# Optimization experiments

Hardware: AMD Instinct MI355X
Metric: run time of the kernel (lower is better)

## Reference

```python
import jax, jax.numpy as jnp
import numpy as np

B, I, H, O, K = 256, 512, 512, 512, 256


def setup_inputs() -> dict:
    key = jax.random.key(0)
    ks = jax.random.split(key, 16)
    def lin(kw, kb, out_dim, in_dim):
        s = 1.0 / np.sqrt(in_dim)
        W = jax.random.uniform(kw, (out_dim, in_dim), jnp.float32, -s, s)
        b = jax.random.uniform(kb, (out_dim,), jnp.float32, -s, s)
        return W, b
    Wd, bd = lin(ks[0], ks[1], H, I + 2 * H)
    Wr, br = lin(ks[2], ks[3], H, I + H)
    Wz, bz = lin(ks[4], ks[5], H, I + H)
    Wh, bh = lin(ks[6], ks[7], H, I + H)
    Wo, bo = lin(ks[8], ks[9], O, H)
    return {
        "sample": jax.random.normal(ks[10], (B, I), jnp.float32),
        "hidden": jax.random.normal(ks[11], (B, H), jnp.float32),
        "hidden_tensor": jax.random.normal(ks[12], (K, B, H), jnp.float32),
        "d_0": jax.random.normal(ks[13], (B, H), jnp.float32),
        "Wd": Wd, "bd": bd, "Wr": Wr, "br": br,
        "Wz": Wz, "bz": bz, "Wh": Wh, "bh": bh, "Wo": Wo, "bo": bo,
    }


def _filter_d(hidden_tensor, d_values):
    # get_ws: w[j] = prod_{m=0}^{K-1-j} (m - d) / (m + 1)  for j in [0, K)
    # Vectorized: cumprod of (m-d)/(m+1) along m, then flip.
    m = jnp.arange(K, dtype=d_values.dtype).reshape(K, 1, 1)  # [K,1,1]
    factors = (m - d_values[None, :, :]) / (m + 1.0)          # [K,B,H]
    w = jnp.flip(jnp.cumprod(factors, axis=0), axis=0)        # [K,B,H]
    return jnp.sum(hidden_tensor * w, axis=0)                 # [B,H]


def reference(sample, hidden, hidden_tensor, d_0,
              Wd, bd, Wr, br, Wz, bz, Wh, bh, Wo, bo):
    combined = jnp.concatenate([sample, hidden], axis=1)          # [B, I+H]
    combined_d = jnp.concatenate([sample, hidden, d_0], axis=1)   # [B, I+2H]

    d_values = jax.nn.sigmoid(combined_d @ Wd.T + bd) * 0.5       # [B,H]
    first = -_filter_d(hidden_tensor, d_values)                   # [B,H]

    r_gate = jax.nn.sigmoid(combined @ Wr.T + br)
    z_gate = jax.nn.sigmoid(combined @ Wz.T + bz)

    combined2 = jnp.concatenate([sample, r_gate * hidden], axis=1)
    h_tilde = jnp.tanh(combined2 @ Wh.T + bh)
    second = h_tilde * (1.0 - z_gate)

    hidden_new = first + second                                   # [B,H]
    h_c_1 = jnp.concatenate([hidden_tensor, hidden_new[None]], axis=0)[1:]  # [K,B,H]
    output = hidden_new @ Wo.T + bo                               # [B,O]
    return (output, hidden_new, h_c_1, d_values)
```

## Files before the change

### kernel.cpp

```cpp
#include <hip/hip_runtime.h>

#define B_ 256
#define H_ 512
#define KF 256
#define BH 131072
#define BH4 32768
#define H4 128

#define BM 64
#define BN 64
#define BK 16

__device__ __forceinline__ float sigmoidf_(float x) { return 1.0f / (1.0f + __expf(-x)); }
__device__ __forceinline__ float tanh_fast(float x) { return 2.0f / (1.0f + __expf(-2.0f * x)) - 1.0f; }
__device__ __forceinline__ float4 sig4(float4 v) {
    return make_float4(sigmoidf_(v.x), sigmoidf_(v.y), sigmoidf_(v.z), sigmoidf_(v.w));
}

#define MAC_LOOP()                                                         \
    _Pragma("unroll")                                                      \
    for (int kk = 0; kk < BK; ++kk) {                                      \
        const float4 a = *(const float4*)&As[kk][ty << 2];                 \
        const float4 w = *(const float4*)&Ws[kk][tx << 2];                 \
        const float a4[4] = {a.x, a.y, a.z, a.w};                          \
        const float w4[4] = {w.x, w.y, w.z, w.w};                          \
        _Pragma("unroll")                                                  \
        for (int i = 0; i < 4; ++i)                                        \
            _Pragma("unroll")                                              \
            for (int j = 0; j < 4; ++j)                                    \
                acc[i][j] = fmaf(a4[i], w4[j], acc[i][j]);                 \
    }

template<bool MUL>
__device__ __forceinline__ void gemm64(
    float (*As)[BM + 4], float (*Ws)[BN + 4],
    const float* __restrict__ abase, const float* __restrict__ rbase,
    const float* __restrict__ W, int Ktot, int ks,
    int bm, int bn, int nIter, float* __restrict__ p)
{
    const int tid = threadIdx.x;
    const int ty = tid >> 4, tx = tid & 15;
    const int lrow = tid >> 2, lcol = (tid & 3) << 2;
    const float* aptr = abase + (bm + lrow) * 512 + lcol;
    const float* rptr = MUL ? rbase + (bm + lrow) * 512 + lcol : nullptr;
    const float* wptr = W + (size_t)(bn + lrow) * Ktot + ks + lcol;

    float acc[4][4] = {};
    float4 av = *(const float4*)aptr;
    if (MUL) { const float4 rv = *(const float4*)rptr;
               av.x *= rv.x; av.y *= rv.y; av.z *= rv.z; av.w *= rv.w; }
    float4 wv = *(const float4*)wptr;

    for (int it = 0; it < nIter; ++it) {
        __syncthreads();
        As[lcol + 0][lrow] = av.x; As[lcol + 1][lrow] = av.y;
        As[lcol + 2][lrow] = av.z; As[lcol + 3][lrow] = av.w;
        Ws[lcol + 0][lrow] = wv.x; Ws[lcol + 1][lrow] = wv.y;
        Ws[lcol + 2][lrow] = wv.z; Ws[lcol + 3][lrow] = wv.w;
        __syncthreads();
        if (it < nIter - 1) {
            av = *(const float4*)(aptr + (it + 1) * BK);
            if (MUL) { const float4 rv = *(const float4*)(rptr + (it + 1) * BK);
                       av.x *= rv.x; av.y *= rv.y; av.z *= rv.z; av.w *= rv.w; }
            wv = *(const float4*)(wptr + (it + 1) * BK);
        }
        MAC_LOOP();
    }
    #pragma unroll
    for (int i = 0; i < 4; ++i) {
        const int m = bm + (ty << 2) + i;
        #pragma unroll
        for (int j = 0; j < 4; ++j)
            p[m * 512 + bn + (tx << 2) + j] = acc[i][j];
    }
}

__device__ __forceinline__ void gemm64_rmul(
    float (*As)[BM + 4], float (*Ws)[BN + 4],
    const float* __restrict__ hidden, const float* __restrict__ rparts,
    const float* __restrict__ br, const float* __restrict__ W,
    int ks, int bm, int bn, float* __restrict__ p)
{
    const int tid = threadIdx.x;
    const int ty = tid >> 4, tx = tid & 15;
    const int lrow = tid >> 2, lcol = (tid & 3) << 2;
    const int off = ks - 512;
    const float* aptr = hidden + (bm + lrow) * 512 + off + lcol;
    const float* rptr = rparts + (bm + lrow) * 512 + off + lcol;
    const float* bptr = br + off + lcol;
    const float* wptr = W + (size_t)(bn + lrow) * 1024 + ks + lcol;

    float acc[4][4] = {};
    float4 av, wv;
    {
        float4 rs = *(const float4*)bptr;
        #pragma unroll
        for (int s = 0; s < 4; ++s) { const float4 rp = *(const float4*)(rptr + (size_t)s * BH);
            rs.x += rp.x; rs.y += rp.y; rs.z += rp.z; rs.w += rp.w; }
        const float4 hv = *(const float4*)aptr;
        av = make_float4(sigmoidf_(rs.x) * hv.x, sigmoidf_(rs.y) * hv.y,
                         sigmoidf_(rs.z) * hv.z, sigmoidf_(rs.w) * hv.w);
        wv = *(const float4*)wptr;
    }
    for (int it = 0; it < 16; ++it) {
        __syncthreads();
        As[lcol + 0][lrow] = av.x; As[lcol + 1][lrow] = av.y;
        As[lcol + 2][lrow] = av.z; As[lcol + 3][lrow] = av.w;
        Ws[lcol + 0][lrow] = wv.x; Ws[lcol + 1][lrow] = wv.y;
        Ws[lcol + 2][lrow] = wv.z; Ws[lcol + 3][lrow] = wv.w;
        __syncthreads();
        if (it < 15) {
            float4 rs = *(const float4*)(bptr + (it + 1) * BK);
            #pragma unroll
            for (int s = 0; s < 4; ++s) { const float4 rp = *(const float4*)(rptr + (size_t)s * BH + (it + 1) * BK);
                rs.x += rp.x; rs.y += rp.y; rs.z += rp.z; rs.w += rp.w; }
            const float4 hv = *(const float4*)(aptr + (it + 1) * BK);
            av = make_float4(sigmoidf_(rs.x) * hv.x, sigmoidf_(rs.y) * hv.y,
                             sigmoidf_(rs.z) * hv.z, sigmoidf_(rs.w) * hv.w);
            wv = *(const float4*)(wptr + (it + 1) * BK);
        }
        MAC_LOOP();
    }
    #pragma unroll
    for (int i = 0; i < 4; ++i) {
        const int m = bm + (ty << 2) + i;
        #pragma unroll
        for (int j = 0; j < 4; ++j)
            p[m * 512 + bn + (tx << 2) + j] = acc[i][j];
    }
}

__global__ __launch_bounds__(256) void k_gemm_drz(
    const float* __restrict__ sample, const float* __restrict__ hidden,
    const float* __restrict__ d0,
    const float* __restrict__ Wd, const float* __restrict__ Wr,
    const float* __restrict__ Wz,
    float* __restrict__ dbase, float* __restrict__ rzbase)
{
    __shared__ float As[BK][BM + 4];
    __shared__ float Ws[BK][BN + 4];
    const int z = blockIdx.z;
    if (z < 6) {
        const int ks = z << 8, seg = ks >> 9;
        const float* ab = (seg == 0 ? sample : (seg == 1 ? hidden : d0)) + (ks & 511);
        gemm64<false>(As, Ws, ab, nullptr, Wd, 1536, ks,
                      blockIdx.y * BM, blockIdx.x * BN, 16, dbase + (size_t)z * BH);
    } else {
        const int id = z - 6, gz = id >> 2, s = id & 3, ks = s << 8;
        const float* ab = (ks < 512 ? sample + ks : hidden + (ks - 512));
        gemm64<false>(As, Ws, ab, nullptr, gz ? Wz : Wr, 1024, ks,
                      blockIdx.y * BM, blockIdx.x * BN, 16, rzbase + (size_t)id * BH);
    }
}

__global__ __launch_bounds__(256) void k_mega(
    const float* __restrict__ ht, const float* __restrict__ bd,
    const float* __restrict__ sample, const float* __restrict__ hidden,
    const float* __restrict__ rparts, const float* __restrict__ br,
    const float* __restrict__ Wh, float* __restrict__ hparts,
    float* hc1, float* __restrict__ dv_out)
{
    if (blockIdx.x < 128) {
        __shared__ float As[BK][BM + 4];
        __shared__ float Ws[BK][BN + 4];
        const int id = blockIdx.x;
        const int s = id >> 5, t2 = id & 31;
        const int bn = (t2 >> 2) << 6, bm = (t2 & 3) << 6, ks = s << 8;
        if (ks < 512)
            gemm64<false>(As, Ws, sample + ks, nullptr, Wh, 1024, ks, bm, bn, 16,
                          hparts + (size_t)s * BH);
        else
            gemm64_rmul(As, Ws, hidden, rparts, br, Wh, ks, bm, bn,
                        hparts + (size_t)s * BH);
        return;
    }
    __shared__ float s_inv[KF], s_tinv[KF];
    const int tid = threadIdx.x;
    const float fi = 1.0f / (float)(tid + 1);
    s_inv[tid] = fi; s_tinv[tid] = (float)tid * fi;
    __syncthreads();

    const int g = (blockIdx.x - 128) * 256 + tid;
    const int n = g & (H_ - 1);
    float sd = bd[n];
    #pragma unroll
    for (int s = 0; s < 6; ++s) sd += hc1[(size_t)s * BH + g];
    const float d = 0.5f * sigmoidf_(sd);
    dv_out[g] = d;

    float c = 1.0f, acc = 0.0f;
    #pragma unroll 16
    for (int t = 0; t < KF; ++t) {
        const int k = KF - 1 - t;
        const float v = ht[(size_t)k * BH + g];
        c *= fmaf(-d, s_inv[t], s_tinv[t]);
        acc = fmaf(v, c, acc);
        if (k >= 1) hc1[(size_t)(k - 1) * BH + g] = v;
    }
    hc1[(size_t)(KF - 1) * BH + g] = acc;
}

__global__ __launch_bounds__(256) void k_finalize(
    const float4* __restrict__ zparts, const float4* __restrict__ bz,
    const float4* __restrict__ hparts, const float4* __restrict__ bh,
    float4* hc1_4, float4* __restrict__ hn_out)
{
    const int g = blockIdx.x * 256 + threadIdx.x;
    const int n = g & (H4 - 1);
    float4 zs = bz[n], hs = bh[n];
    #pragma unroll
    for (int s = 0; s < 4; ++s) { const float4 p = zparts[(size_t)s * BH4 + g];
        zs.x += p.x; zs.y += p.y; zs.z += p.z; zs.w += p.w; }
    #pragma unroll
    for (int s = 0; s < 4; ++s) { const float4 p = hparts[(size_t)s * BH4 + g];
        hs.x += p.x; hs.y += p.y; hs.z += p.z; hs.w += p.w; }
    const float4 z = sig4(zs);
    const float4 a = hc1_4[(size_t)255 * BH4 + g];
    float4 hn;
    hn.x = tanh_fast(hs.x) * (1.0f - z.x) - a.x;
    hn.y = tanh_fast(hs.y) * (1.0f - z.y) - a.y;
    hn.z = tanh_fast(hs.z) * (1.0f - z.z) - a.z;
    hn.w = tanh_fast(hs.w) * (1.0f - z.w) - a.w;
    hn_out[g] = hn;
    hc1_4[(size_t)255 * BH4 + g] = hn;
}

__global__ __launch_bounds__(256) void k_gemm_o(
    const float* __restrict__ hn, const float* __restrict__ Wo,
    float* __restrict__ parts, int chunk)
{
    __shared__ float As[BK][BM + 4];
    __shared__ float Ws[BK][BN + 4];
    const int s = blockIdx.z, ks = s * chunk;
    gemm64<false>(As, Ws, hn + ks, nullptr, Wo, 512, ks,
                  blockIdx.y * BM, blockIdx.x * BN, chunk / BK, parts + (size_t)s * BH);
}

__global__ __launch_bounds__(256) void k_reduce_o(
    const float4* parts, const float4* __restrict__ bo, float4* out, int NS)
{
    const int g = blockIdx.x * 256 + threadIdx.x;
    float4 v = bo[g & (H4 - 1)];
    for (int s = 0; s < NS; ++s) { const float4 p = parts[(size_t)s * BH4 + g];
        v.x += p.x; v.y += p.y; v.z += p.z; v.w += p.w; }
    out[g] = v;
}

__global__ __launch_bounds__(256) void k_reduce_rz(
    const float4* __restrict__ parts, const float4* __restrict__ br,
    const float4* __restrict__ bz, float4* __restrict__ rb, float4* __restrict__ zb)
{
    const int g = blockIdx.x * 256 + threadIdx.x;
    const int n = g & (H4 - 1);
    float4 r = br[n], z = bz[n];
    #pragma unroll
    for (int s = 0; s < 4; ++s) { const float4 p = parts[(size_t)s * BH4 + g];
        r.x += p.x; r.y += p.y; r.z += p.z; r.w += p.w; }
    #pragma unroll
    for (int s = 4; s < 8; ++s) { const float4 p = parts[(size_t)s * BH4 + g];
        z.x += p.x; z.y += p.y; z.z += p.z; z.w += p.w; }
    rb[g] = sig4(r); zb[g] = sig4(z);
}

__global__ __launch_bounds__(256) void k_gemm_h(
    const float* __restrict__ sample, const float* __restrict__ hidden,
    const float* __restrict__ rb, const float* __restrict__ Wh,
    float* __restrict__ parts)
{
    __shared__ float As[BK][BM + 4];
    __shared__ float Ws[BK][BN + 4];
    const int s = blockIdx.z, ks = s << 8;
    if (ks < 512)
        gemm64<false>(As, Ws, sample + ks, nullptr, Wh, 1024, ks,
                      blockIdx.y * BM, blockIdx.x * BN, 16, parts + (size_t)s * BH);
    else
        gemm64<true>(As, Ws, hidden + (ks - 512), rb + (ks - 512), Wh, 1024, ks,
                     blockIdx.y * BM, blockIdx.x * BN, 16, parts + (size_t)s * BH);
}

__global__ __launch_bounds__(256) void k_filter_full(
    const float* __restrict__ ht, const float* dparts, const float* __restrict__ bd,
    const float* zbuf, const float* hparts, const float* __restrict__ bh,
    float* hc1, float* __restrict__ dv_out, float* __restrict__ hn_out)
{
    __shared__ float s_inv[KF], s_tinv[KF];
    const int tid = threadIdx.x;
    const float fi = 1.0f / (float)(tid + 1);
    s_inv[tid] = fi; s_tinv[tid] = (float)tid * fi;
    __syncthreads();

    const int g = blockIdx.x * 256 + tid;
    const int n = g & (H_ - 1);
    float sd = bd[n];
    #pragma unroll
    for (int s = 0; s < 6; ++s) sd += dparts[(size_t)s * BH + g];
    const float d = 0.5f * sigmoidf_(sd);
    dv_out[g] = d;
    float sh = bh[n];
    #pragma unroll
    for (int s = 0; s < 4; ++s) sh += hparts[(size_t)s * BH + g];
    const float z = zbuf[g];

    float c = 1.0f, acc = 0.0f;
    #pragma unroll 16
    for (int t = 0; t < KF; ++t) {
        const int k = KF - 1 - t;
        const float v = ht[(size_t)k * BH + g];
        c *= fmaf(-d, s_inv[t], s_tinv[t]);
        acc = fmaf(v, c, acc);
        if (k >= 1) hc1[(size_t)(k - 1) * BH + g] = v;
    }
    const float hn = tanh_fast(sh) * (1.0f - z) - acc;
    hc1[(size_t)(KF - 1) * BH + g] = hn;
    hn_out[g] = hn;
}

extern "C" void kernel_launch(void* const* d_in, const int* in_sizes, int n_in,
                              void* d_out, int out_size, void* d_ws, size_t ws_size,
                              hipStream_t stream)
{
    const float* sample = (const float*)d_in[0];
    const float* hidden = (const float*)d_in[1];
    const float* ht     = (const float*)d_in[2];
    const float* d0     = (const float*)d_in[3];
    const float* Wd = (const float*)d_in[4];
    const float* bd = (const float*)d_in[5];
    const float* Wr = (const float*)d_in[6];
    const float* br = (const float*)d_in[7];
    const float* Wz = (const float*)d_in[8];
    const float* bz = (const float*)d_in[9];
    const float* Wh = (const float*)d_in[10];
    const float* bh = (const float*)d_in[11];
    const float* Wo = (const float*)d_in[12];
    const float* bo = (const float*)d_in[13];

    float* out     = (float*)d_out;
    float* out_o   = out;
    float* out_hn  = out + BH;
    float* out_hc1 = out + 2 * BH;
    float* out_dv  = out + 2 * BH + (size_t)KF * BH;

    const size_t slice = BH;
    const size_t need = 12ull * slice * sizeof(float);

    if (ws_size >= need) {
        float* ws = (float*)d_ws;
        k_gemm_drz<<<dim3(8, 4, 14), 256, 0, stream>>>(sample, hidden, d0,
                                                       Wd, Wr, Wz, out_hc1, ws);
        k_mega<<<dim3(640), 256, 0, stream>>>(ht, bd, sample, hidden,
                                              ws , br, Wh,
                                              ws + 8 * slice ,
                                              out_hc1, out_dv);
        k_finalize<<<dim3(128), 256, 0, stream>>>(
            (const float4*)(ws + 4 * slice), (const float4*)bz,
            (const float4*)(ws + 8 * slice), (const float4*)bh,
            (float4*)out_hc1, (float4*)out_hn);
        k_gemm_o<<<dim3(8, 4, 4), 256, 0, stream>>>(out_hn, Wo, ws, 128);
        k_reduce_o<<<dim3(128), 256, 0, stream>>>((const float4*)ws,
                                                  (const float4*)bo,
                                                  (float4*)out_o, 4);
    } else {
        float* sl = out_hc1;
        k_gemm_drz<<<dim3(8, 4, 14), 256, 0, stream>>>(sample, hidden, d0,
                                                       Wd, Wr, Wz, sl, sl + 6 * slice);
        k_reduce_rz<<<dim3(128), 256, 0, stream>>>((const float4*)(sl + 6 * slice),
                                                   (const float4*)br, (const float4*)bz,
                                                   (float4*)(sl + 14 * slice),
                                                   (float4*)(sl + 15 * slice));
        k_gemm_h<<<dim3(8, 4, 4), 256, 0, stream>>>(sample, hidden, sl + 14 * slice, Wh,
                                                    sl + 16 * slice);
        k_filter_full<<<dim3(512), 256, 0, stream>>>(ht, sl, bd, sl + 15 * slice,
                                                     sl + 16 * slice, bh,
                                                     out_hc1, out_dv, out_hn);
        k_gemm_o<<<dim3(8, 4, 1), 256, 0, stream>>>(out_hn, Wo, out_o, 512);
        k_reduce_o<<<dim3(128), 256, 0, stream>>>((const float4*)out_o, (const float4*)bo,
                                                  (float4*)out_o, 1);
    }
}
```

Before: 92.79 us.

## Split fractional filter scan into segments and precompute gate activations

The 256-step sequential filter recurrence is split into four 64-step segments, each computed by separate blocks on two elements per thread. The finalize kernel recombines the segments using prefix products of the weight recurrence, which it recomputes per element. A new small kernel reduces the d/r/z partial sums and applies the sigmoids up front, so the Wh GEMM can use the generic multiply path instead of recomputing the r gate per tile. The aim is more memory-level parallelism on the bandwidth-bound history copy and scan. The cost is an extra launch and redundant prefix-product work in finalize.

```diff
diff --git a/kernel.cpp b/kernel.cpp
--- a/kernel.cpp
+++ b/kernel.cpp
@@ -4,6 +4,7 @@
 #define H_ 512
 #define KF 256
 #define BH 131072
+#define BH2 65536
 #define BH4 32768
 #define H4 128
 
@@ -75,61 +76,6 @@
     }
 }
 
-__device__ __forceinline__ void gemm64_rmul(
-    float (*As)[BM + 4], float (*Ws)[BN + 4],
-    const float* __restrict__ hidden, const float* __restrict__ rparts,
-    const float* __restrict__ br, const float* __restrict__ W,
-    int ks, int bm, int bn, float* __restrict__ p)
-{
-    const int tid = threadIdx.x;
-    const int ty = tid >> 4, tx = tid & 15;
-    const int lrow = tid >> 2, lcol = (tid & 3) << 2;
-    const int off = ks - 512;
-    const float* aptr = hidden + (bm + lrow) * 512 + off + lcol;
-    const float* rptr = rparts + (bm + lrow) * 512 + off + lcol;
-    const float* bptr = br + off + lcol;
-    const float* wptr = W + (size_t)(bn + lrow) * 1024 + ks + lcol;
-
-    float acc[4][4] = {};
-    float4 av, wv;
-    {
-        float4 rs = *(const float4*)bptr;
-        #pragma unroll
-        for (int s = 0; s < 4; ++s) { const float4 rp = *(const float4*)(rptr + (size_t)s * BH);
-            rs.x += rp.x; rs.y += rp.y; rs.z += rp.z; rs.w += rp.w; }
-        const float4 hv = *(const float4*)aptr;
-        av = make_float4(sigmoidf_(rs.x) * hv.x, sigmoidf_(rs.y) * hv.y,
-                         sigmoidf_(rs.z) * hv.z, sigmoidf_(rs.w) * hv.w);
-        wv = *(const float4*)wptr;
-    }
-    for (int it = 0; it < 16; ++it) {
-        __syncthreads();
-        As[lcol + 0][lrow] = av.x; As[lcol + 1][lrow] = av.y;
-        As[lcol + 2][lrow] = av.z; As[lcol + 3][lrow] = av.w;
-        Ws[lcol + 0][lrow] = wv.x; Ws[lcol + 1][lrow] = wv.y;
-        Ws[lcol + 2][lrow] = wv.z; Ws[lcol + 3][lrow] = wv.w;
-        __syncthreads();
-        if (it < 15) {
-            float4 rs = *(const float4*)(bptr + (it + 1) * BK);
-            #pragma unroll
-            for (int s = 0; s < 4; ++s) { const float4 rp = *(const float4*)(rptr + (size_t)s * BH + (it + 1) * BK);
-                rs.x += rp.x; rs.y += rp.y; rs.z += rp.z; rs.w += rp.w; }
-            const float4 hv = *(const float4*)(aptr + (it + 1) * BK);
-            av = make_float4(sigmoidf_(rs.x) * hv.x, sigmoidf_(rs.y) * hv.y,
-                             sigmoidf_(rs.z) * hv.z, sigmoidf_(rs.w) * hv.w);
-            wv = *(const float4*)(wptr + (it + 1) * BK);
-        }
-        MAC_LOOP();
-    }
-    #pragma unroll
-    for (int i = 0; i < 4; ++i) {
-        const int m = bm + (ty << 2) + i;
-        #pragma unroll
-        for (int j = 0; j < 4; ++j)
-            p[m * 512 + bn + (tx << 2) + j] = acc[i][j];
-    }
-}
-
 __global__ __launch_bounds__(256) void k_gemm_drz(
     const float* __restrict__ sample, const float* __restrict__ hidden,
     const float* __restrict__ d0,
@@ -153,12 +99,35 @@
     }
 }
 
+__global__ __launch_bounds__(256) void k_dv(
+    const float4* __restrict__ dparts, const float4* __restrict__ bd,
+    const float4* __restrict__ rzparts, const float4* __restrict__ br,
+    const float4* __restrict__ bz,
+    float4* __restrict__ dv4, float4* __restrict__ rb4, float4* __restrict__ zb4)
+{
+    const int g = blockIdx.x * 256 + threadIdx.x;
+    const int n = g & (H4 - 1);
+    float4 sd = bd[n], sr = br[n], sz = bz[n];
+    #pragma unroll
+    for (int s = 0; s < 6; ++s) { const float4 p = dparts[(size_t)s * BH4 + g];
+        sd.x += p.x; sd.y += p.y; sd.z += p.z; sd.w += p.w; }
+    #pragma unroll
+    for (int s = 0; s < 4; ++s) { const float4 p = rzparts[(size_t)s * BH4 + g];
+        sr.x += p.x; sr.y += p.y; sr.z += p.z; sr.w += p.w; }
+    #pragma unroll
+    for (int s = 4; s < 8; ++s) { const float4 p = rzparts[(size_t)s * BH4 + g];
+        sz.x += p.x; sz.y += p.y; sz.z += p.z; sz.w += p.w; }
+    const float4 d = sig4(sd);
+    dv4[g] = make_float4(0.5f * d.x, 0.5f * d.y, 0.5f * d.z, 0.5f * d.w);
+    rb4[g] = sig4(sr);
+    zb4[g] = sig4(sz);
+}
+
 __global__ __launch_bounds__(256) void k_mega(
-    const float* __restrict__ ht, const float* __restrict__ bd,
+    const float2* __restrict__ ht2, const float2* __restrict__ dv2,
     const float* __restrict__ sample, const float* __restrict__ hidden,
-    const float* __restrict__ rparts, const float* __restrict__ br,
-    const float* __restrict__ Wh, float* __restrict__ hparts,
-    float* hc1, float* __restrict__ dv_out)
+    const float* __restrict__ rb, const float* __restrict__ Wh,
+    float* __restrict__ ws, float2* __restrict__ hc12)
 {
     if (blockIdx.x < 128) {
         __shared__ float As[BK][BM + 4];
@@ -168,10 +137,10 @@
         const int bn = (t2 >> 2) << 6, bm = (t2 & 3) << 6, ks = s << 8;
         if (ks < 512)
             gemm64<false>(As, Ws, sample + ks, nullptr, Wh, 1024, ks, bm, bn, 16,
-                          hparts + (size_t)s * BH);
+                          ws + (size_t)s * BH);
         else
-            gemm64_rmul(As, Ws, hidden, rparts, br, Wh, ks, bm, bn,
-                        hparts + (size_t)s * BH);
+            gemm64<true>(As, Ws, hidden + (ks - 512), rb + (ks - 512), Wh, 1024, ks,
+                         bm, bn, 16, ws + (size_t)s * BH);
         return;
     }
     __shared__ float s_inv[KF], s_tinv[KF];
@@ -180,47 +149,85 @@
     s_inv[tid] = fi; s_tinv[tid] = (float)tid * fi;
     __syncthreads();
 
-    const int g = (blockIdx.x - 128) * 256 + tid;
-    const int n = g & (H_ - 1);
-    float sd = bd[n];
-    #pragma unroll
-    for (int s = 0; s < 6; ++s) sd += hc1[(size_t)s * BH + g];
-    const float d = 0.5f * sigmoidf_(sd);
-    dv_out[g] = d;
-
-    float c = 1.0f, acc = 0.0f;
-    #pragma unroll 16
-    for (int t = 0; t < KF; ++t) {
-        const int k = KF - 1 - t;
-        const float v = ht[(size_t)k * BH + g];
-        c *= fmaf(-d, s_inv[t], s_tinv[t]);
-        acc = fmaf(v, c, acc);
-        if (k >= 1) hc1[(size_t)(k - 1) * BH + g] = v;
-    }
-    hc1[(size_t)(KF - 1) * BH + g] = acc;
+    const int fb  = blockIdx.x - 128;
+    const int seg = fb >> 8;
+    const int cp  = ((fb & 255) << 8) | tid;
+    const float2 d2 = dv2[cp];
+    const int t0 = seg << 6;
+
+    float c0 = 1.0f, c1 = 1.0f, a0 = 0.0f, a1 = 0.0f;
+    #pragma unroll 16
+    for (int i = 0; i < 64; ++i) {
+        const int t = t0 + i;
+        const int k = 255 - t;
+        const float2 v = ht2[(size_t)k * BH2 + cp];
+        const float iv = s_inv[t], tv = s_tinv[t];
+        c0 *= fmaf(-d2.x, iv, tv);
+        c1 *= fmaf(-d2.y, iv, tv);
+        a0 = fmaf(v.x, c0, a0);
+        a1 = fmaf(v.y, c1, a1);
+        if (k >= 1) hc12[(size_t)(k - 1) * BH2 + cp] = v;
+    }
+    ((float2*)ws)[(size_t)(4 + seg) * BH2 + cp] = make_float2(a0, a1);
 }
 
 __global__ __launch_bounds__(256) void k_finalize(
-    const float4* __restrict__ zparts, const float4* __restrict__ bz,
-    const float4* __restrict__ hparts, const float4* __restrict__ bh,
+    const float4* __restrict__ dv4, const float4* __restrict__ ws4,
+    const float4* __restrict__ bh, const float4* __restrict__ zb4,
     float4* hc1_4, float4* __restrict__ hn_out)
 {
-    const int g = blockIdx.x * 256 + threadIdx.x;
+    __shared__ float s_inv[192], s_tinv[192];
+    const int tid = threadIdx.x;
+    if (tid < 192) { const float fi = 1.0f / (float)(tid + 1);
+                     s_inv[tid] = fi; s_tinv[tid] = (float)tid * fi; }
+    __syncthreads();
+
+    const int g = blockIdx.x * 256 + tid;
     const int n = g & (H4 - 1);
-    float4 zs = bz[n], hs = bh[n];
-    #pragma unroll
-    for (int s = 0; s < 4; ++s) { const float4 p = zparts[(size_t)s * BH4 + g];
-        zs.x += p.x; zs.y += p.y; zs.z += p.z; zs.w += p.w; }
-    #pragma unroll
-    for (int s = 0; s < 4; ++s) { const float4 p = hparts[(size_t)s * BH4 + g];
+    const float4 d = dv4[g];
+
+    float4 c = make_float4(1.f, 1.f, 1.f, 1.f), px0, px1, px2;
+    #pragma unroll 16
+    for (int t = 0; t < 64; ++t) {
+        const float iv = s_inv[t], tv = s_tinv[t];
+        c.x *= fmaf(-d.x, iv, tv); c.y *= fmaf(-d.y, iv, tv);
+        c.z *= fmaf(-d.z, iv, tv); c.w *= fmaf(-d.w, iv, tv);
+    }
+    px0 = c;
+    #pragma unroll 16
+    for (int t = 64; t < 128; ++t) {
+        const float iv = s_inv[t], tv = s_tinv[t];
+        c.x *= fmaf(-d.x, iv, tv); c.y *= fmaf(-d.y, iv, tv);
+        c.z *= fmaf(-d.z, iv, tv); c.w *= fmaf(-d.w, iv, tv);
+    }
+    px1 = c;
+    #pragma unroll 16
+    for (int t = 128; t < 192; ++t) {
+        const float iv = s_inv[t], tv = s_tinv[t];
+        c.x *= fmaf(-d.x, iv, tv); c.y *= fmaf(-d.y, iv, tv);
+        c.z *= fmaf(-d.z, iv, tv); c.w *= fmaf(-d.w, iv, tv);
+    }
+    px2 = c;
+
+    const float4 a0 = ws4[(size_t)4 * BH4 + g];
+    const float4 a1 = ws4[(size_t)5 * BH4 + g];
+    const float4 a2 = ws4[(size_t)6 * BH4 + g];
+    const float4 a3 = ws4[(size_t)7 * BH4 + g];
+    float4 hs = bh[n];
+    #pragma unroll
+    for (int s = 0; s < 4; ++s) { const float4 p = ws4[(size_t)s * BH4 + g];
         hs.x += p.x; hs.y += p.y; hs.z += p.z; hs.w += p.w; }
-    const float4 z = sig4(zs);
-    const float4 a = hc1_4[(size_t)255 * BH4 + g];
+    const float4 z = zb4[g];
+
     float4 hn;
-    hn.x = tanh_fast(hs.x) * (1.0f - z.x) - a.x;
-    hn.y = tanh_fast(hs.y) * (1.0f - z.y) - a.y;
-    hn.z = tanh_fast(hs.z) * (1.0f - z.z) - a.z;
-    hn.w = tanh_fast(hs.w) * (1.0f - z.w) - a.w;
+    hn.x = tanh_fast(hs.x) * (1.0f - z.x)
+         - (a0.x + px0.x * a1.x + px1.x * a2.x + px2.x * a3.x);
+    hn.y = tanh_fast(hs.y) * (1.0f - z.y)
+         - (a0.y + px0.y * a1.y + px1.y * a2.y + px2.y * a3.y);
+    hn.z = tanh_fast(hs.z) * (1.0f - z.z)
+         - (a0.z + px0.z * a1.z + px1.z * a2.z + px2.z * a3.z);
+    hn.w = tanh_fast(hs.w) * (1.0f - z.w)
+         - (a0.w + px0.w * a1.w + px1.w * a2.w + px2.w * a3.w);
     hn_out[g] = hn;
     hc1_4[(size_t)255 * BH4 + g] = hn;
 }
@@ -341,19 +348,25 @@
     float* out_dv  = out + 2 * BH + (size_t)KF * BH;
 
     const size_t slice = BH;
-    const size_t need = 12ull * slice * sizeof(float);
+    const size_t need = 10ull * slice * sizeof(float);
 
     if (ws_size >= need) {
         float* ws = (float*)d_ws;
+        float* rb = ws + 8 * slice;
+        float* zb = ws + 9 * slice;
+
         k_gemm_drz<<<dim3(8, 4, 14), 256, 0, stream>>>(sample, hidden, d0,
                                                        Wd, Wr, Wz, out_hc1, ws);
-        k_mega<<<dim3(640), 256, 0, stream>>>(ht, bd, sample, hidden,
-                                              ws , br, Wh,
-                                              ws + 8 * slice ,
-                                              out_hc1, out_dv);
+        k_dv<<<dim3(128), 256, 0, stream>>>(
+            (const float4*)out_hc1, (const float4*)bd,
+            (const float4*)ws, (const float4*)br, (const float4*)bz,
+            (float4*)out_dv, (float4*)rb, (float4*)zb);
+        k_mega<<<dim3(1152), 256, 0, stream>>>(
+            (const float2*)ht, (const float2*)out_dv, sample, hidden, rb, Wh,
+            ws, (float2*)out_hc1);
         k_finalize<<<dim3(128), 256, 0, stream>>>(
-            (const float4*)(ws + 4 * slice), (const float4*)bz,
-            (const float4*)(ws + 8 * slice), (const float4*)bh,
+            (const float4*)out_dv, (const float4*)ws,
+            (const float4*)bh, (const float4*)zb,
             (float4*)out_hc1, (float4*)out_hn);
         k_gemm_o<<<dim3(8, 4, 4), 256, 0, stream>>>(out_hn, Wo, ws, 128);
         k_reduce_o<<<dim3(128), 256, 0, stream>>>((const float4*)ws,
```

New measurement: 109.6 us. 18.1% more time.
